# Optimization experiments

Hardware: AMD Instinct MI355X
Metric: run time of the kernel (lower is better)

The kernel has to match this reference:

```python
import jax, jax.numpy as jnp
import numpy as np

CH, G, K, STRIDE, RR = 256, 16, 7, 1, 4
GROUP = CH // G            # channels per group
PAD = (K - 1) // 2
BN_EPS = 1e-5


def setup_inputs() -> dict:
    key = jax.random.key(0)
    ks = jax.random.split(key, 9)
    b, dim = 16, 4096
    hid = CH // RR  # 64
    return {
        "x": jax.random.normal(ks[0], (b, CH, dim), jnp.float32),
        "w1": jax.random.normal(ks[1], (hid, CH), jnp.float32) * (1.0 / np.sqrt(CH)),
        "b1": jax.random.normal(ks[2], (hid,), jnp.float32) * 0.02,
        "bn_gamma": 1.0 + 0.1 * jax.random.normal(ks[3], (hid,), jnp.float32),
        "bn_beta": 0.1 * jax.random.normal(ks[4], (hid,), jnp.float32),
        "bn_mean": 0.1 * jax.random.normal(ks[5], (hid,), jnp.float32),
        "bn_var": jax.random.uniform(ks[6], (hid,), jnp.float32) + 0.5,
        "w2": jax.random.normal(ks[7], (K * G, hid), jnp.float32) * (1.0 / np.sqrt(hid)),
        "b2": jax.random.normal(ks[8], (K * G,), jnp.float32) * 0.02,
    }


def _involution(x, w1, b1, bn_gamma, bn_beta, bn_mean, bn_var, w2, b2):
    b, ch, dim = x.shape
    L = dim // STRIDE  # out_dim
    # unfold: pad then gather K shifted strided views -> [b, ch, K, L]
    xp = jnp.pad(x, ((0, 0), (0, 0), (PAD, PAD)))
    unfolded = jnp.stack(
        [xp[:, :, k : k + STRIDE * (L - 1) + 1 : STRIDE] for k in range(K)], axis=2
    )
    unfolded = unfolded.reshape(b, G, GROUP, K, L)
    # adaptive max pool to L (windows of size STRIDE); identity when STRIDE == 1
    pooled = x.reshape(b, ch, L, STRIDE).max(axis=-1)
    # kernel generator: 1x1 conv -> relu -> batchnorm (inference) -> 1x1 conv
    h = jnp.einsum("oc,bcl->bol", w1, pooled) + b1[:, None]
    h = jax.nn.relu(h)
    h = (h - bn_mean[:, None]) * jax.lax.rsqrt(bn_var[:, None] + BN_EPS)
    h = h * bn_gamma[:, None] + bn_beta[:, None]
    kern = jnp.einsum("oc,bcl->bol", w2, h) + b2[:, None]  # [b, K*G, L]
    kern = kern.reshape(b, G, K, L)
    # per-location dynamic kernel multiply + reduce over K
    out = jnp.einsum("bgkl,bgckl->bgcl", kern, unfolded)
    return out.reshape(b, ch, L)


def reference(x, w1, b1, bn_gamma, bn_beta, bn_mean, bn_var, w2, b2):
    return _involution(x, w1, b1, bn_gamma, bn_beta, bn_mean, bn_var, w2, b2)
```

## Files before the change

### kernel.cpp

```cpp
#include <hip/hip_runtime.h>

#define BB   16
#define CHN  256
#define DIMN 4096
#define KK   7
#define PADK 3
#define HID  64
#define KGN  112
#define TLC  64
#define XSD  35
#define XSH  70
#define HSTH 70
#define KSTD 68
#define BN_EPS 1e-5f

typedef __fp16 half2_t __attribute__((ext_vector_type(2)));
typedef __fp16 half8   __attribute__((ext_vector_type(8)));
typedef float  f32x4   __attribute__((ext_vector_type(4)));

union U32H2 { unsigned int u; half2_t h; };

static __device__ __forceinline__ unsigned int packf(float a, float b) {
    U32H2 t; t.h = __builtin_amdgcn_cvt_pkrtz(a, b); return t.u;
}
static __device__ __forceinline__ half2_t ash2(unsigned int u) { U32H2 t; t.u = u; return t.h; }
static __device__ __forceinline__ __fp16 u16h(unsigned short u) {
    return __builtin_bit_cast(__fp16, u);
}
static __device__ __forceinline__ unsigned short hu16(__fp16 h) {
    return __builtin_bit_cast(unsigned short, h);
}

__global__ __launch_bounds__(256) void setup_k(
    const float* __restrict__ w1, const float* __restrict__ w2,
    const float* __restrict__ bn_gamma, const float* __restrict__ bn_beta,
    const float* __restrict__ bn_mean,  const float* __restrict__ bn_var,
    __fp16* __restrict__ w1f, __fp16* __restrict__ w2f,
    float* __restrict__ scb, float* __restrict__ shb) {
    int t = blockIdx.x * 256 + threadIdx.x;
    if (t < HID * CHN) w1f[t] = (__fp16)w1[t];
    if (t < KGN * HID) w2f[t] = (__fp16)w2[t];
    if (t < HID) {
        float s = bn_gamma[t] * rsqrtf(bn_var[t] + BN_EPS);
        scb[t] = s;
        shb[t] = bn_beta[t] - bn_mean[t] * s;
    }
}

template <int OFF>
static __device__ __forceinline__ void extract_kv(const uint4 q[4], float kv[KK][4]) {
#pragma unroll
    for (int k = 0; k < KK; ++k) {
        const int kk = k + OFF;
        const int i  = kk >> 1;
        const int h  = kk & 1;
#pragma unroll
        for (int j = 0; j < 4; ++j) {
            unsigned int u = (&q[i].x)[j];
            half2_t hh = ash2(u);
            kv[k][j] = h ? (float)hh[1] : (float)hh[0];
        }
    }
}

__global__ __launch_bounds__(256, 3) void fused_k(
    const float* __restrict__ x,
    const __fp16* __restrict__ w1f,
    const float* __restrict__ b1,
    const float* __restrict__ scb, const float* __restrict__ shb,
    const __fp16* __restrict__ w2f,
    const float* __restrict__ b2,
    float* __restrict__ out) {
    __shared__ unsigned int xs[CHN * XSD];
    __shared__ unsigned int un[56 * KSTD];

    unsigned short* xs16 = (unsigned short*)xs;
    unsigned short* hs16 = (unsigned short*)un;
    unsigned int*   ks   = un;

    const int t    = threadIdx.x;
    const int lane = t & 63;
    const int w    = t >> 6;
    const int lr   = t & 15;
    const int lg   = (t >> 4) & 3;
    const int b    = blockIdx.x >> 6;
    const int l0   = (blockIdx.x & 63) * TLC;
    const int colL = 16 * w + lr;

    {
        const int colq = t & 15;
        const int chl  = t >> 4;
        const float* xg = x + ((size_t)b * CHN + chl) * DIMN + l0 + 4 * colq;
        float4 v[16];
#pragma unroll
        for (int i = 0; i < 16; ++i)
            v[i] = *(const float4*)(xg + (size_t)(16 * i) * DIMN);
#pragma unroll
        for (int i = 0; i < 16; ++i) {
            unsigned short* rp = xs16 + (chl + 16 * i) * XSH + 4 * colq + 3;
            rp[0] = hu16((__fp16)v[i].x);
            *(unsigned int*)(rp + 1) = packf(v[i].y, v[i].z);
            rp[3] = hu16((__fp16)v[i].w);
        }
        const float* xrow = x + ((size_t)b * CHN + t) * DIMN;
        float4 lv = (l0 > 0) ? *(const float4*)(xrow + l0 - 4)
                             : make_float4(0.f, 0.f, 0.f, 0.f);
        float4 rv = (l0 + TLC < DIMN) ? *(const float4*)(xrow + l0 + TLC)
                                      : make_float4(0.f, 0.f, 0.f, 0.f);
        unsigned short* hp = xs16 + t * XSH;
        hp[0]  = hu16((__fp16)lv.y);
        hp[1]  = hu16((__fp16)lv.z);
        hp[2]  = hu16((__fp16)lv.w);
        hp[67] = hu16((__fp16)rv.x);
        hp[68] = hu16((__fp16)rv.y);
        hp[69] = hu16((__fp16)rv.z);
    }
    __syncthreads();

    f32x4 acc[4];
#pragma unroll
    for (int of = 0; of < 4; ++of) acc[of] = (f32x4){0.f, 0.f, 0.f, 0.f};

#pragma unroll
    for (int p = 0; p < 8; ++p) {
        half8 bf;
#pragma unroll
        for (int j = 0; j < 8; ++j)
            bf[j] = u16h(xs16[(32 * p + 8 * lg + j) * XSH + colL + 3]);
#pragma unroll
        for (int of = 0; of < 4; ++of) {
            half8 af = *(const half8*)(w1f + (16 * of + lr) * CHN + 32 * p + 8 * lg);
            acc[of] = __builtin_amdgcn_mfma_f32_16x16x32_f16(af, bf, acc[of], 0, 0, 0);
        }
    }

#pragma unroll
    for (int of = 0; of < 4; ++of) {
#pragma unroll
        for (int r = 0; r < 4; ++r) {
            const int o = 16 * of + 4 * lg + r;
            float hv = fmaxf(acc[of][r] + b1[o], 0.f) * scb[o] + shb[o];
            hs16[o * HSTH + colL] = hu16((__fp16)hv);
        }
    }

    f32x4 acc2[7];
#pragma unroll
    for (int rf = 0; rf < 7; ++rf) acc2[rf] = (f32x4){0.f, 0.f, 0.f, 0.f};

#pragma unroll
    for (int kx = 0; kx < 2; ++kx) {
        half8 bf;
#pragma unroll
        for (int j = 0; j < 8; ++j)
            bf[j] = u16h(hs16[(32 * kx + 8 * lg + j) * HSTH + colL]);
#pragma unroll
        for (int rf = 0; rf < 7; ++rf) {
            half8 af = *(const half8*)(w2f + (16 * rf + lr) * HID + 32 * kx + 8 * lg);
            acc2[rf] = __builtin_amdgcn_mfma_f32_16x16x32_f16(af, bf, acc2[rf], 0, 0, 0);
        }
    }

    __syncthreads();

#pragma unroll
    for (int rf = 0; rf < 7; ++rf) {
#pragma unroll
        for (int p = 0; p < 2; ++p) {
            const int r0 = 16 * rf + 4 * lg + 2 * p;
            float k0 = acc2[rf][2 * p + 0] + b2[r0 + 0];
            float k1 = acc2[rf][2 * p + 1] + b2[r0 + 1];
            ks[(r0 >> 1) * KSTD + colL] = packf(k0, k1);
        }
    }
    __syncthreads();

    const int q4    = lane & 15;
    const int hi    = lane >> 4;
    const int cbase = 4 * q4;

#pragma unroll
    for (int gi = 0; gi < 4; ++gi) {
        const int g   = 4 * w + gi;
        const int rpb = (7 * g) >> 1;
        uint4 qq[4];
#pragma unroll
        for (int ii = 0; ii < 4; ++ii)
            qq[ii] = *(const uint4*)(ks + (rpb + ii) * KSTD + cbase);
        float kv[KK][4];
        if ((g & 1) == 0) extract_kv<0>(qq, kv);
        else              extract_kv<1>(qq, kv);

#pragma unroll
        for (int i2 = 0; i2 < 4; ++i2) {
            const int ch = 16 * g + 4 * i2 + hi;
            const unsigned int* xr = xs + ch * XSD + (cbase >> 1);
            unsigned int uu[5];
#pragma unroll
            for (int j = 0; j < 5; ++j) uu[j] = xr[j];
            float xv[10];
#pragma unroll
            for (int r = 0; r < 10; ++r) {
                half2_t hh = ash2(uu[r >> 1]);
                xv[r] = (r & 1) ? (float)hh[1] : (float)hh[0];
            }
            float o0 = 0.f, o1 = 0.f, o2 = 0.f, o3 = 0.f;
#pragma unroll
            for (int k = 0; k < KK; ++k) {
                o0 = fmaf(kv[k][0], xv[k + 0], o0);
                o1 = fmaf(kv[k][1], xv[k + 1], o1);
                o2 = fmaf(kv[k][2], xv[k + 2], o2);
                o3 = fmaf(kv[k][3], xv[k + 3], o3);
            }
            *(float4*)(out + ((size_t)b * CHN + ch) * DIMN + l0 + cbase) =
                make_float4(o0, o1, o2, o3);
        }
    }
}

extern "C" void kernel_launch(void* const* d_in, const int* in_sizes, int n_in,
                              void* d_out, int out_size, void* d_ws, size_t ws_size,
                              hipStream_t stream) {
    (void)in_sizes; (void)n_in; (void)out_size; (void)ws_size;

    const float* x        = (const float*)d_in[0];
    const float* w1       = (const float*)d_in[1];
    const float* b1       = (const float*)d_in[2];
    const float* bn_gamma = (const float*)d_in[3];
    const float* bn_beta  = (const float*)d_in[4];
    const float* bn_mean  = (const float*)d_in[5];
    const float* bn_var   = (const float*)d_in[6];
    const float* w2       = (const float*)d_in[7];
    const float* b2       = (const float*)d_in[8];
    float*       out      = (float*)d_out;

    __fp16* w1f = (__fp16*)d_ws;
    __fp16* w2f = w1f + HID * CHN;
    float*  scb = (float*)(w2f + KGN * HID);
    float*  shb = scb + HID;

    setup_k<<<(HID * CHN + 255) / 256, 256, 0, stream>>>(
        w1, w2, bn_gamma, bn_beta, bn_mean, bn_var, w1f, w2f, scb, shb);
    fused_k<<<BB * (DIMN / TLC), 256, 0, stream>>>(
        x, w1f, b1, scb, shb, w2f, b2, out);
}
```

Measured before the change: 55.90 us.

## Make fused kernel process four tiles per block with double-buffered prefetch

```diff
diff --git a/kernel.cpp b/kernel.cpp
--- a/kernel.cpp
+++ b/kernel.cpp
@@ -4,10 +4,10 @@
 #define CHN  256
 #define DIMN 4096
 #define KK   7
-#define PADK 3
 #define HID  64
 #define KGN  112
 #define TLC  64
+#define NT   4
 #define XSD  35
 #define XSH  70
 #define HSTH 70
@@ -29,6 +29,12 @@
 }
 static __device__ __forceinline__ unsigned short hu16(__fp16 h) {
     return __builtin_bit_cast(unsigned short, h);
+}
+
+static __device__ __forceinline__ void bar_lds() {
+    asm volatile("s_waitcnt lgkmcnt(0)" ::: "memory");
+    __builtin_amdgcn_s_barrier();
+    __builtin_amdgcn_sched_barrier(0);
 }
 
 __global__ __launch_bounds__(256) void setup_k(
@@ -63,7 +69,41 @@
     }
 }
 
-__global__ __launch_bounds__(256, 3) void fused_k(
+static __device__ __forceinline__ void load_tile(
+    const float* __restrict__ x, int b, int l0, int colq, int chl, int trow,
+    float4 v[16], float4& lv, float4& rv) {
+    const float* xg = x + ((size_t)b * CHN + chl) * DIMN + l0 + 4 * colq;
+#pragma unroll
+    for (int i = 0; i < 16; ++i)
+        v[i] = *(const float4*)(xg + (size_t)(16 * i) * DIMN);
+    const float* xrow = x + ((size_t)b * CHN + trow) * DIMN;
+    lv = (l0 > 0) ? *(const float4*)(xrow + l0 - 4)
+                  : make_float4(0.f, 0.f, 0.f, 0.f);
+    rv = (l0 + TLC < DIMN) ? *(const float4*)(xrow + l0 + TLC)
+                           : make_float4(0.f, 0.f, 0.f, 0.f);
+}
+
+static __device__ __forceinline__ void store_tile(
+    unsigned int* xs, int colq, int chl, int trow,
+    const float4 v[16], const float4 lv, const float4 rv) {
+    unsigned short* xs16 = (unsigned short*)xs;
+#pragma unroll
+    for (int i = 0; i < 16; ++i) {
+        unsigned short* rp = xs16 + (chl + 16 * i) * XSH + 4 * colq + 3;
+        rp[0] = hu16((__fp16)v[i].x);
+        *(unsigned int*)(rp + 1) = packf(v[i].y, v[i].z);
+        rp[3] = hu16((__fp16)v[i].w);
+    }
+    unsigned short* hp = xs16 + trow * XSH;
+    hp[0]  = hu16((__fp16)lv.y);
+    hp[1]  = hu16((__fp16)lv.z);
+    hp[2]  = hu16((__fp16)lv.w);
+    hp[67] = hu16((__fp16)rv.x);
+    hp[68] = hu16((__fp16)rv.y);
+    hp[69] = hu16((__fp16)rv.z);
+}
+
+__global__ __launch_bounds__(256, 1) void fused_k(
     const float* __restrict__ x,
     const __fp16* __restrict__ w1f,
     const float* __restrict__ b1,
@@ -71,149 +111,139 @@
     const __fp16* __restrict__ w2f,
     const float* __restrict__ b2,
     float* __restrict__ out) {
-    __shared__ unsigned int xs[CHN * XSD];
-    __shared__ unsigned int un[56 * KSTD];
-
-    unsigned short* xs16 = (unsigned short*)xs;
-    unsigned short* hs16 = (unsigned short*)un;
-    unsigned int*   ks   = un;
+    __shared__ unsigned int   xs0[CHN * XSD];
+    __shared__ unsigned int   xs1[CHN * XSD];
+    __shared__ unsigned short hsb[HID * HSTH];
+    __shared__ unsigned int   ksb[56 * KSTD];
 
     const int t    = threadIdx.x;
     const int lane = t & 63;
     const int w    = t >> 6;
     const int lr   = t & 15;
     const int lg   = (t >> 4) & 3;
-    const int b    = blockIdx.x >> 6;
-    const int l0   = (blockIdx.x & 63) * TLC;
     const int colL = 16 * w + lr;
+    const int colq = t & 15;
+    const int chl  = t >> 4;
+
+    float4 v[16], lv, rv;
 
     {
-        const int colq = t & 15;
-        const int chl  = t >> 4;
-        const float* xg = x + ((size_t)b * CHN + chl) * DIMN + l0 + 4 * colq;
-        float4 v[16];
-#pragma unroll
-        for (int i = 0; i < 16; ++i)
-            v[i] = *(const float4*)(xg + (size_t)(16 * i) * DIMN);
-#pragma unroll
-        for (int i = 0; i < 16; ++i) {
-            unsigned short* rp = xs16 + (chl + 16 * i) * XSH + 4 * colq + 3;
-            rp[0] = hu16((__fp16)v[i].x);
-            *(unsigned int*)(rp + 1) = packf(v[i].y, v[i].z);
-            rp[3] = hu16((__fp16)v[i].w);
-        }
-        const float* xrow = x + ((size_t)b * CHN + t) * DIMN;
-        float4 lv = (l0 > 0) ? *(const float4*)(xrow + l0 - 4)
-                             : make_float4(0.f, 0.f, 0.f, 0.f);
-        float4 rv = (l0 + TLC < DIMN) ? *(const float4*)(xrow + l0 + TLC)
-                                      : make_float4(0.f, 0.f, 0.f, 0.f);
-        unsigned short* hp = xs16 + t * XSH;
-        hp[0]  = hu16((__fp16)lv.y);
-        hp[1]  = hu16((__fp16)lv.z);
-        hp[2]  = hu16((__fp16)lv.w);
-        hp[67] = hu16((__fp16)rv.x);
-        hp[68] = hu16((__fp16)rv.y);
-        hp[69] = hu16((__fp16)rv.z);
-    }
-    __syncthreads();
-
-    f32x4 acc[4];
-#pragma unroll
-    for (int of = 0; of < 4; ++of) acc[of] = (f32x4){0.f, 0.f, 0.f, 0.f};
-
-#pragma unroll
-    for (int p = 0; p < 8; ++p) {
-        half8 bf;
-#pragma unroll
-        for (int j = 0; j < 8; ++j)
-            bf[j] = u16h(xs16[(32 * p + 8 * lg + j) * XSH + colL + 3]);
+        const int tid0 = blockIdx.x * NT;
+        load_tile(x, tid0 >> 6, (tid0 & 63) * TLC, colq, chl, t, v, lv, rv);
+    }
+
+#pragma unroll 2
+    for (int tt = 0; tt < NT; ++tt) {
+        const int ctid = blockIdx.x * NT + tt;
+        const int b    = ctid >> 6;
+        const int l0   = (ctid & 63) * TLC;
+        unsigned int*   xs   = (tt & 1) ? xs1 : xs0;
+        unsigned short* xs16 = (unsigned short*)xs;
+
+        store_tile(xs, colq, chl, t, v, lv, rv);
+
+        if (tt + 1 < NT) {
+            const int ntid = ctid + 1;
+            load_tile(x, ntid >> 6, (ntid & 63) * TLC, colq, chl, t, v, lv, rv);
+        }
+        bar_lds();
+
+        f32x4 acc[4];
+#pragma unroll
+        for (int of = 0; of < 4; ++of) acc[of] = (f32x4){0.f, 0.f, 0.f, 0.f};
+
+#pragma unroll
+        for (int p = 0; p < 8; ++p) {
+            half8 bf;
+#pragma unroll
+            for (int j = 0; j < 8; ++j)
+                bf[j] = u16h(xs16[(32 * p + 8 * lg + j) * XSH + colL + 3]);
+#pragma unroll
+            for (int of = 0; of < 4; ++of) {
+                half8 af = *(const half8*)(w1f + (16 * of + lr) * CHN + 32 * p + 8 * lg);
+                acc[of] = __builtin_amdgcn_mfma_f32_16x16x32_f16(af, bf, acc[of], 0, 0, 0);
+            }
+        }
+
 #pragma unroll
         for (int of = 0; of < 4; ++of) {
-            half8 af = *(const half8*)(w1f + (16 * of + lr) * CHN + 32 * p + 8 * lg);
-            acc[of] = __builtin_amdgcn_mfma_f32_16x16x32_f16(af, bf, acc[of], 0, 0, 0);
-        }
-    }
-
-#pragma unroll
-    for (int of = 0; of < 4; ++of) {
-#pragma unroll
-        for (int r = 0; r < 4; ++r) {
-            const int o = 16 * of + 4 * lg + r;
-            float hv = fmaxf(acc[of][r] + b1[o], 0.f) * scb[o] + shb[o];
-            hs16[o * HSTH + colL] = hu16((__fp16)hv);
-        }
-    }
-
-    f32x4 acc2[7];
-#pragma unroll
-    for (int rf = 0; rf < 7; ++rf) acc2[rf] = (f32x4){0.f, 0.f, 0.f, 0.f};
-
-#pragma unroll
-    for (int kx = 0; kx < 2; ++kx) {
-        half8 bf;
-#pragma unroll
-        for (int j = 0; j < 8; ++j)
-            bf[j] = u16h(hs16[(32 * kx + 8 * lg + j) * HSTH + colL]);
+#pragma unroll
+            for (int r = 0; r < 4; ++r) {
+                const int o = 16 * of + 4 * lg + r;
+                float hv = fmaxf(acc[of][r] + b1[o], 0.f) * scb[o] + shb[o];
+                hsb[o * HSTH + colL] = hu16((__fp16)hv);
+            }
+        }
+
+        f32x4 acc2[7];
+#pragma unroll
+        for (int rf = 0; rf < 7; ++rf) acc2[rf] = (f32x4){0.f, 0.f, 0.f, 0.f};
+
+#pragma unroll
+        for (int kx = 0; kx < 2; ++kx) {
+            half8 bf;
+#pragma unroll
+            for (int j = 0; j < 8; ++j)
+                bf[j] = u16h(hsb[(32 * kx + 8 * lg + j) * HSTH + colL]);
+#pragma unroll
+            for (int rf = 0; rf < 7; ++rf) {
+                half8 af = *(const half8*)(w2f + (16 * rf + lr) * HID + 32 * kx + 8 * lg);
+                acc2[rf] = __builtin_amdgcn_mfma_f32_16x16x32_f16(af, bf, acc2[rf], 0, 0, 0);
+            }
+        }
+
 #pragma unroll
         for (int rf = 0; rf < 7; ++rf) {
-            half8 af = *(const half8*)(w2f + (16 * rf + lr) * HID + 32 * kx + 8 * lg);
-            acc2[rf] = __builtin_amdgcn_mfma_f32_16x16x32_f16(af, bf, acc2[rf], 0, 0, 0);
-        }
-    }
-
-    __syncthreads();
-
-#pragma unroll
-    for (int rf = 0; rf < 7; ++rf) {
-#pragma unroll
-        for (int p = 0; p < 2; ++p) {
-            const int r0 = 16 * rf + 4 * lg + 2 * p;
-            float k0 = acc2[rf][2 * p + 0] + b2[r0 + 0];
-            float k1 = acc2[rf][2 * p + 1] + b2[r0 + 1];
-            ks[(r0 >> 1) * KSTD + colL] = packf(k0, k1);
-        }
-    }
-    __syncthreads();
-
-    const int q4    = lane & 15;
-    const int hi    = lane >> 4;
-    const int cbase = 4 * q4;
-
-#pragma unroll
-    for (int gi = 0; gi < 4; ++gi) {
-        const int g   = 4 * w + gi;
-        const int rpb = (7 * g) >> 1;
-        uint4 qq[4];
-#pragma unroll
-        for (int ii = 0; ii < 4; ++ii)
-            qq[ii] = *(const uint4*)(ks + (rpb + ii) * KSTD + cbase);
-        float kv[KK][4];
-        if ((g & 1) == 0) extract_kv<0>(qq, kv);
-        else              extract_kv<1>(qq, kv);
-
-#pragma unroll
-        for (int i2 = 0; i2 < 4; ++i2) {
-            const int ch = 16 * g + 4 * i2 + hi;
-            const unsigned int* xr = xs + ch * XSD + (cbase >> 1);
-            unsigned int uu[5];
-#pragma unroll
-            for (int j = 0; j < 5; ++j) uu[j] = xr[j];
-            float xv[10];
-#pragma unroll
-            for (int r = 0; r < 10; ++r) {
-                half2_t hh = ash2(uu[r >> 1]);
-                xv[r] = (r & 1) ? (float)hh[1] : (float)hh[0];
-            }
-            float o0 = 0.f, o1 = 0.f, o2 = 0.f, o3 = 0.f;
-#pragma unroll
-            for (int k = 0; k < KK; ++k) {
-                o0 = fmaf(kv[k][0], xv[k + 0], o0);
-                o1 = fmaf(kv[k][1], xv[k + 1], o1);
-                o2 = fmaf(kv[k][2], xv[k + 2], o2);
-                o3 = fmaf(kv[k][3], xv[k + 3], o3);
-            }
-            *(float4*)(out + ((size_t)b * CHN + ch) * DIMN + l0 + cbase) =
-                make_float4(o0, o1, o2, o3);
+#pragma unroll
+            for (int p2 = 0; p2 < 2; ++p2) {
+                const int r0 = 16 * rf + 4 * lg + 2 * p2;
+                float k0 = acc2[rf][2 * p2 + 0] + b2[r0 + 0];
+                float k1 = acc2[rf][2 * p2 + 1] + b2[r0 + 1];
+                ksb[(r0 >> 1) * KSTD + colL] = packf(k0, k1);
+            }
+        }
+        bar_lds();
+
+        const int q4    = lane & 15;
+        const int hi    = lane >> 4;
+        const int cbase = 4 * q4;
+
+#pragma unroll
+        for (int gi = 0; gi < 4; ++gi) {
+            const int g   = 4 * w + gi;
+            const int rpb = (7 * g) >> 1;
+            uint4 qq[4];
+#pragma unroll
+            for (int ii = 0; ii < 4; ++ii)
+                qq[ii] = *(const uint4*)(ksb + (rpb + ii) * KSTD + cbase);
+            float kv[KK][4];
+            if ((gi & 1) == 0) extract_kv<0>(qq, kv);
+            else               extract_kv<1>(qq, kv);
+
+#pragma unroll
+            for (int i2 = 0; i2 < 4; ++i2) {
+                const int ch = 16 * g + 4 * i2 + hi;
+                const unsigned int* xr = xs + ch * XSD + (cbase >> 1);
+                unsigned int uu[5];
+#pragma unroll
+                for (int j = 0; j < 5; ++j) uu[j] = xr[j];
+                float xv[10];
+#pragma unroll
+                for (int r = 0; r < 10; ++r) {
+                    half2_t hh = ash2(uu[r >> 1]);
+                    xv[r] = (r & 1) ? (float)hh[1] : (float)hh[0];
+                }
+                float o0 = 0.f, o1 = 0.f, o2 = 0.f, o3 = 0.f;
+#pragma unroll
+                for (int k = 0; k < KK; ++k) {
+                    o0 = fmaf(kv[k][0], xv[k + 0], o0);
+                    o1 = fmaf(kv[k][1], xv[k + 1], o1);
+                    o2 = fmaf(kv[k][2], xv[k + 2], o2);
+                    o3 = fmaf(kv[k][3], xv[k + 3], o3);
+                }
+                *(float4*)(out + ((size_t)b * CHN + ch) * DIMN + l0 + cbase) =
+                    make_float4(o0, o1, o2, o3);
+            }
         }
     }
 }
@@ -241,6 +271,6 @@
 
     setup_k<<<(HID * CHN + 255) / 256, 256, 0, stream>>>(
         w1, w2, bn_gamma, bn_beta, bn_mean, bn_var, w1f, w2f, scb, shb);
-    fused_k<<<BB * (DIMN / TLC), 256, 0, stream>>>(
+    fused_k<<<(BB * (DIMN / TLC)) / NT, 256, 0, stream>>>(
         x, w1f, b1, scb, shb, w2f, b2, out);
 }
```

Result: slower. 83.30 us (+49.0%).

## Pipeline x tile loads with first MFMA stage using double-buffered registers

Applied to the files above, without the earlier changes.

```diff
diff --git a/kernel.cpp b/kernel.cpp
--- a/kernel.cpp
+++ b/kernel.cpp
@@ -4,7 +4,6 @@
 #define CHN  256
 #define DIMN 4096
 #define KK   7
-#define PADK 3
 #define HID  64
 #define KGN  112
 #define TLC  64
@@ -29,6 +28,12 @@
 }
 static __device__ __forceinline__ unsigned short hu16(__fp16 h) {
     return __builtin_bit_cast(unsigned short, h);
+}
+
+static __device__ __forceinline__ void bar_lds() {
+    asm volatile("s_waitcnt lgkmcnt(0)" ::: "memory");
+    __builtin_amdgcn_s_barrier();
+    __builtin_amdgcn_sched_barrier(0);
 }
 
 __global__ __launch_bounds__(256) void setup_k(
@@ -87,26 +92,46 @@
     const int l0   = (blockIdx.x & 63) * TLC;
     const int colL = 16 * w + lr;
 
+    const int colq = t & 15;
+    const int chl  = t >> 4;
+    const float* xgb = x + (size_t)b * CHN * DIMN + l0 + 4 * colq;
+
+    float4 vA[2], vB[2];
+
+#define LOADP(P, V)                                                          \
+    { _Pragma("unroll")                                                      \
+      for (int i = 0; i < 2; ++i)                                            \
+          V[i] = *(const float4*)(xgb + (size_t)(32 * (P) + chl + 16 * i) * DIMN); }
+
+#define WRITEP(P, V)                                                         \
+    { _Pragma("unroll")                                                      \
+      for (int i = 0; i < 2; ++i) {                                          \
+          const int row = 32 * (P) + chl + 16 * i;                           \
+          unsigned short* rp = xs16 + row * XSH + 4 * colq + 3;              \
+          rp[0] = hu16((__fp16)V[i].x);                                      \
+          *(unsigned int*)(rp + 1) = packf(V[i].y, V[i].z);                  \
+          rp[3] = hu16((__fp16)V[i].w);                                      \
+      } }
+
+#define KSTEP(P)                                                             \
+    { half8 bf;                                                              \
+      _Pragma("unroll")                                                      \
+      for (int j = 0; j < 8; ++j)                                            \
+          bf[j] = u16h(xs16[(32 * (P) + 8 * lg + j) * XSH + colL + 3]);      \
+      _Pragma("unroll")                                                      \
+      for (int of = 0; of < 4; ++of) {                                       \
+          half8 af = *(const half8*)(w1f + (16 * of + lr) * CHN + 32 * (P) + 8 * lg); \
+          acc[of] = __builtin_amdgcn_mfma_f32_16x16x32_f16(af, bf, acc[of], 0, 0, 0); \
+      } }
+
+    LOADP(0, vA);
     {
-        const int colq = t & 15;
-        const int chl  = t >> 4;
-        const float* xg = x + ((size_t)b * CHN + chl) * DIMN + l0 + 4 * colq;
-        float4 v[16];
-#pragma unroll
-        for (int i = 0; i < 16; ++i)
-            v[i] = *(const float4*)(xg + (size_t)(16 * i) * DIMN);
-#pragma unroll
-        for (int i = 0; i < 16; ++i) {
-            unsigned short* rp = xs16 + (chl + 16 * i) * XSH + 4 * colq + 3;
-            rp[0] = hu16((__fp16)v[i].x);
-            *(unsigned int*)(rp + 1) = packf(v[i].y, v[i].z);
-            rp[3] = hu16((__fp16)v[i].w);
-        }
         const float* xrow = x + ((size_t)b * CHN + t) * DIMN;
         float4 lv = (l0 > 0) ? *(const float4*)(xrow + l0 - 4)
                              : make_float4(0.f, 0.f, 0.f, 0.f);
         float4 rv = (l0 + TLC < DIMN) ? *(const float4*)(xrow + l0 + TLC)
                                       : make_float4(0.f, 0.f, 0.f, 0.f);
+        WRITEP(0, vA);
         unsigned short* hp = xs16 + t * XSH;
         hp[0]  = hu16((__fp16)lv.y);
         hp[1]  = hu16((__fp16)lv.z);
@@ -115,24 +140,21 @@
         hp[68] = hu16((__fp16)rv.y);
         hp[69] = hu16((__fp16)rv.z);
     }
-    __syncthreads();
+    LOADP(1, vB);
+    bar_lds();
 
     f32x4 acc[4];
 #pragma unroll
     for (int of = 0; of < 4; ++of) acc[of] = (f32x4){0.f, 0.f, 0.f, 0.f};
 
-#pragma unroll
-    for (int p = 0; p < 8; ++p) {
-        half8 bf;
-#pragma unroll
-        for (int j = 0; j < 8; ++j)
-            bf[j] = u16h(xs16[(32 * p + 8 * lg + j) * XSH + colL + 3]);
-#pragma unroll
-        for (int of = 0; of < 4; ++of) {
-            half8 af = *(const half8*)(w1f + (16 * of + lr) * CHN + 32 * p + 8 * lg);
-            acc[of] = __builtin_amdgcn_mfma_f32_16x16x32_f16(af, bf, acc[of], 0, 0, 0);
-        }
-    }
+    KSTEP(0); WRITEP(1, vB); LOADP(2, vA); bar_lds();
+    KSTEP(1); WRITEP(2, vA); LOADP(3, vB); bar_lds();
+    KSTEP(2); WRITEP(3, vB); LOADP(4, vA); bar_lds();
+    KSTEP(3); WRITEP(4, vA); LOADP(5, vB); bar_lds();
+    KSTEP(4); WRITEP(5, vB); LOADP(6, vA); bar_lds();
+    KSTEP(5); WRITEP(6, vA); LOADP(7, vB); bar_lds();
+    KSTEP(6); WRITEP(7, vB);               bar_lds();
+    KSTEP(7);
 
 #pragma unroll
     for (int of = 0; of < 4; ++of) {
@@ -161,7 +183,7 @@
         }
     }
 
-    __syncthreads();
+    bar_lds();
 
 #pragma unroll
     for (int rf = 0; rf < 7; ++rf) {
@@ -173,7 +195,7 @@
             ks[(r0 >> 1) * KSTD + colL] = packf(k0, k1);
         }
     }
-    __syncthreads();
+    bar_lds();
 
     const int q4    = lane & 15;
     const int hi    = lane >> 4;
@@ -188,7 +210,7 @@
         for (int ii = 0; ii < 4; ++ii)
             qq[ii] = *(const uint4*)(ks + (rpb + ii) * KSTD + cbase);
         float kv[KK][4];
-        if ((g & 1) == 0) extract_kv<0>(qq, kv);
+        if ((gi & 1) == 0) extract_kv<0>(qq, kv);
         else              extract_kv<1>(qq, kv);
 
 #pragma unroll
@@ -216,6 +238,9 @@
                 make_float4(o0, o1, o2, o3);
         }
     }
+#undef LOADP
+#undef WRITEP
+#undef KSTEP
 }
 
 extern "C" void kernel_launch(void* const* d_in, const int* in_sizes, int n_in,
```

New measurement: 58.56 us. 4.8% more time.
